# Kernel tuning notes

Measured on AMD Instinct MI355X. Metric: run time of the kernel, lower is better.

## Reference

```python
import jax, jax.numpy as jnp
import numpy as np

DT = 0.001  # integration time step (forward arg dt in the original module)


def force_fn(x):
    # Harmonic well stand-in for the user-supplied force function.
    return -x


def _nh_step(x, v, alpha, kT, mass, Q):
    """One Nose-Hoover step, exactly mirroring the recompute block in backward()."""
    ndof = x.shape[-1]
    v2 = (v * v).sum(-1)
    alpha = alpha + (DT / 4) * (v2 - ndof * kT) / Q
    v = v * jnp.exp(-alpha[..., None] * (DT / 2))
    v2 = (v * v).sum(-1)
    alpha = alpha + (DT / 4) * (v2 - ndof * kT) / Q
    v = v + (DT / 2) * force_fn(x) / mass
    x = x + DT * v
    v = v + (DT / 2) * force_fn(x) / mass
    v2 = (v * v).sum(-1)
    alpha = alpha + (DT / 4) * (v2 - ndof * kT) / Q
    v = v * jnp.exp(-alpha[..., None] * (DT / 2))
    v2 = (v * v).sum(-1)
    alpha = alpha + (DT / 4) * (v2 - ndof * kT) / Q
    return x, v, alpha


def setup_inputs() -> dict:
    key = jax.random.key(0)
    k1, k2 = jax.random.split(key)
    B, D = 4096, 64  # batch of systems, degrees of freedom per system
    return {
        "x0": jax.random.normal(k1, (B, D), jnp.float32),
        "v0": jax.random.normal(k2, (B, D), jnp.float32),
        "alpha0": jnp.zeros((B,), jnp.float32),
        "kT": jnp.ones((), jnp.float32),
        "mass": jnp.ones((), jnp.float32),
        "Q": jnp.ones((), jnp.float32),
        "n_steps": 1000,
        "store_every": 10,
    }


def reference(x0, v0, alpha0, kT, mass, Q, n_steps, store_every):
    n_chunks = n_steps // store_every  # assume divisibility (1000 / 10)

    def inner(c, _):
        x, v, a = c
        return _nh_step(x, v, a, kT, mass, Q), None

    def chunk(c, _):
        c, _ = jax.lax.scan(inner, c, None, length=store_every)
        return c, (c[0], c[1])  # snapshot (x, v) every store_every steps

    _, (xs, vs) = jax.lax.scan(chunk, (x0, v0, alpha0), None, length=n_chunks)
    traj_x = jnp.concatenate([x0[None], xs], axis=0)  # [n_steps//store_every + 1, B, D]
    traj_v = jnp.concatenate([v0[None], vs], axis=0)
    return traj_x, traj_v
```

## Files before the change

kernel.cpp:

```cpp
#include <hip/hip_runtime.h>

#define DT 0.001f

typedef float f4 __attribute__((ext_vector_type(4)));

template<int CTRL>
__device__ __forceinline__ float dpp_add(float v) {
    int r = __builtin_amdgcn_update_dpp(0, __float_as_int(v), CTRL, 0xf, 0xf, false);
    return v + __int_as_float(r);
}

__device__ __forceinline__ float reduce16(float t) {
    t = dpp_add<0x121>(t);
    t = dpp_add<0x122>(t);
    t = dpp_add<0x124>(t);
    t = dpp_add<0x128>(t);
    return t;
}

__global__ __launch_bounds__(256) void nh_kernel(
    const float* __restrict__ x0, const float* __restrict__ v0,
    const float* __restrict__ alpha0,
    const float* __restrict__ kT_p, const float* __restrict__ mass_p,
    const float* __restrict__ Q_p,
    const int* __restrict__ n_steps_p, const int* __restrict__ store_every_p,
    float* __restrict__ out, int B)
{
    const int D = 64;
    const int gid = blockIdx.x * blockDim.x + threadIdx.x;
    const int sys = gid >> 4;
    const int g   = gid & 15;
    if (sys >= B) return;

    const int n_steps = *n_steps_p;
    const int se      = *store_every_p;
    const int n_chunks = n_steps / se;

    const float kt = *kT_p, m = *mass_p, q = *Q_p;
    const float c   = 0.25f * DT / q;
    const float E   = (float)D * kt;
    const float hd  = 0.5f * DT / m;
    const float hdt = 0.5f * DT;

    const int snap4 = B * 16;
    const int fidx  = sys * 16 + g;

    const f4* x04 = (const f4*)x0;
    const f4* v04 = (const f4*)v0;
    f4 x = x04[fidx];
    f4 v = v04[fidx];
    float alpha = alpha0[sys];

    f4* outx = (f4*)out;
    f4* outv = ((f4*)out) + (size_t)(n_chunks + 1) * snap4;

    __builtin_nontemporal_store(x, &outx[fidx]);
    __builtin_nontemporal_store(v, &outv[fidx]);

    float v2 = reduce16(v.x*v.x + v.y*v.y + v.z*v.z + v.w*v.w);

    for (int ck = 1; ck <= n_chunks; ++ck) {
        for (int s = 0; s < se; ++s) {
            alpha += c * (v2 - E);
            float s1 = __expf(-hdt * alpha);
            v *= s1;
            v2 *= s1 * s1;
            alpha += c * (v2 - E);
            v -= hd * x;
            x += DT * v;
            v -= hd * x;
            float t = v.x*v.x;
            t = fmaf(v.y, v.y, t);
            t = fmaf(v.z, v.z, t);
            t = fmaf(v.w, v.w, t);
            v2 = reduce16(t);
            alpha += c * (v2 - E);
            float s2 = __expf(-hdt * alpha);
            v *= s2;
            v2 *= s2 * s2;
            alpha += c * (v2 - E);
        }
        __builtin_nontemporal_store(x, &outx[(size_t)ck * snap4 + fidx]);
        __builtin_nontemporal_store(v, &outv[(size_t)ck * snap4 + fidx]);
    }
}

extern "C" void kernel_launch(void* const* d_in, const int* in_sizes, int n_in,
                              void* d_out, int out_size, void* d_ws, size_t ws_size,
                              hipStream_t stream) {
    const float* x0     = (const float*)d_in[0];
    const float* v0     = (const float*)d_in[1];
    const float* alpha0 = (const float*)d_in[2];
    const float* kT     = (const float*)d_in[3];
    const float* mass   = (const float*)d_in[4];
    const float* Q      = (const float*)d_in[5];
    const int* n_steps  = (const int*)d_in[6];
    const int* store_ev = (const int*)d_in[7];

    const int B = in_sizes[0] / 64;
    const int threads = B * 16;
    const int block = 256;
    const int grid = (threads + block - 1) / block;

    nh_kernel<<<grid, block, 0, stream>>>(x0, v0, alpha0, kT, mass, Q,
                                          n_steps, store_ev, (float*)d_out, B);
}
```

Before: 296.4 us.

## Fuse adjacent thermostat half-steps, use polynomial exp, specialize store_every=10

Each step's trailing thermostat half-step is merged with the next step's leading one. This removes a separate velocity scaling and alpha update per interior step. Hardware exp is replaced by a cubic Taylor polynomial, which is accurate only while hdt*alpha stays small. A template specialization for store_every==10 lets the inner loop fully unroll. The aim is to shorten the serial per-step dependency chain, at the cost of reduced exp accuracy if alpha grows large.

Measured after the change: 272.4 us. 8.1% less time.

```diff
diff --git a/kernel.cpp b/kernel.cpp
--- a/kernel.cpp
+++ b/kernel.cpp
@@ -16,6 +16,61 @@
     t = dpp_add<0x124>(t);
     t = dpp_add<0x128>(t);
     return t;
+}
+
+__device__ __forceinline__ float expm(float z) {
+    float p = __builtin_fmaf(z, -0.16666667f, 0.5f);
+    p = __builtin_fmaf(z, p, -1.0f);
+    p = __builtin_fmaf(z, p, 1.0f);
+    return p;
+}
+
+__device__ __forceinline__ float sumsq(const f4& v) {
+    float ta = v.x * v.x, tb = v.y * v.y, tc = v.z * v.z, td = v.w * v.w;
+    return (ta + tb) + (tc + td);
+}
+
+template<int SE>
+__device__ __forceinline__ void run(f4& x, f4& v, float& alpha, float& r,
+                                    int n_chunks, int se_rt,
+                                    float c, float cE, float c2E, float hd, float hdt,
+                                    f4* outx, f4* outv, int snap4, int fidx)
+{
+    const int se = (SE > 0) ? SE : se_rt;
+    const float c2 = 2.0f * c;
+    for (int ck = 1; ck <= n_chunks; ++ck) {
+        alpha = __builtin_fmaf(c, r, alpha - cE);
+        float s1 = expm(hdt * alpha);
+        v *= s1;
+        r *= s1 * s1;
+        alpha = __builtin_fmaf(c, r, alpha - cE);
+        #pragma unroll
+        for (int i = 0; i < se - 1; ++i) {
+            v -= hd * x;
+            x += DT * v;
+            v -= hd * x;
+            r = reduce16(sumsq(v));
+            alpha = __builtin_fmaf(c, r, alpha - cE);
+            float s2 = expm(hdt * alpha);
+            r *= s2 * s2;
+            alpha = __builtin_fmaf(c2, r, alpha - c2E);
+            float s1n = expm(hdt * alpha);
+            v *= s2 * s1n;
+            r *= s1n * s1n;
+            alpha = __builtin_fmaf(c, r, alpha - cE);
+        }
+        v -= hd * x;
+        x += DT * v;
+        v -= hd * x;
+        r = reduce16(sumsq(v));
+        alpha = __builtin_fmaf(c, r, alpha - cE);
+        float s2 = expm(hdt * alpha);
+        v *= s2;
+        r *= s2 * s2;
+        alpha = __builtin_fmaf(c, r, alpha - cE);
+        __builtin_nontemporal_store(x, &outx[(size_t)ck * snap4 + fidx]);
+        __builtin_nontemporal_store(v, &outv[(size_t)ck * snap4 + fidx]);
+    }
 }
 
 __global__ __launch_bounds__(256) void nh_kernel(
@@ -39,16 +94,16 @@
     const float kt = *kT_p, m = *mass_p, q = *Q_p;
     const float c   = 0.25f * DT / q;
     const float E   = (float)D * kt;
+    const float cE  = c * E;
+    const float c2E = 2.0f * cE;
     const float hd  = 0.5f * DT / m;
     const float hdt = 0.5f * DT;
 
     const int snap4 = B * 16;
     const int fidx  = sys * 16 + g;
 
-    const f4* x04 = (const f4*)x0;
-    const f4* v04 = (const f4*)v0;
-    f4 x = x04[fidx];
-    f4 v = v04[fidx];
+    f4 x = ((const f4*)x0)[fidx];
+    f4 v = ((const f4*)v0)[fidx];
     float alpha = alpha0[sys];
 
     f4* outx = (f4*)out;
@@ -57,32 +112,12 @@
     __builtin_nontemporal_store(x, &outx[fidx]);
     __builtin_nontemporal_store(v, &outv[fidx]);
 
-    float v2 = reduce16(v.x*v.x + v.y*v.y + v.z*v.z + v.w*v.w);
+    float r = reduce16(sumsq(v));
 
-    for (int ck = 1; ck <= n_chunks; ++ck) {
-        for (int s = 0; s < se; ++s) {
-            alpha += c * (v2 - E);
-            float s1 = __expf(-hdt * alpha);
-            v *= s1;
-            v2 *= s1 * s1;
-            alpha += c * (v2 - E);
-            v -= hd * x;
-            x += DT * v;
-            v -= hd * x;
-            float t = v.x*v.x;
-            t = fmaf(v.y, v.y, t);
-            t = fmaf(v.z, v.z, t);
-            t = fmaf(v.w, v.w, t);
-            v2 = reduce16(t);
-            alpha += c * (v2 - E);
-            float s2 = __expf(-hdt * alpha);
-            v *= s2;
-            v2 *= s2 * s2;
-            alpha += c * (v2 - E);
-        }
-        __builtin_nontemporal_store(x, &outx[(size_t)ck * snap4 + fidx]);
-        __builtin_nontemporal_store(v, &outv[(size_t)ck * snap4 + fidx]);
-    }
+    if (se == 10)
+        run<10>(x, v, alpha, r, n_chunks, se, c, cE, c2E, hd, hdt, outx, outv, snap4, fidx);
+    else
+        run<0>(x, v, alpha, r, n_chunks, se, c, cE, c2E, hd, hdt, outx, outv, snap4, fidx);
 }
 
 extern "C" void kernel_launch(void* const* d_in, const int* in_sizes, int n_in,
```
